# Kernel tuning notes

Measured on AMD Instinct MI355X. Metric: run time of the kernel, lower is better.

The kernel has to match this reference:

```python
import jax, jax.numpy as jnp
import numpy as np

NUM_NODES = 50000
NUM_EDGES = 800000
NUM_FEATS = 128
HIDDEN = 32
HEADS = 4
NUM_GRAPHS = 64
NEG_SLOPE = 0.2


def _glorot(key, shape):
    fan = shape[0] + shape[-1]
    return jax.random.normal(key, shape, jnp.float32) * np.float32(np.sqrt(2.0 / fan))


def setup_inputs() -> dict:
    key = jax.random.key(0)
    ks = jax.random.split(key, 16)
    x = jax.random.normal(ks[0], (NUM_NODES, NUM_FEATS), jnp.float32)
    edge_index = jax.random.randint(ks[1], (2, NUM_EDGES), 0, NUM_NODES, dtype=jnp.int64)
    batch = jnp.sort(jax.random.randint(ks[2], (NUM_NODES,), 0, NUM_GRAPHS, dtype=jnp.int64))
    d1 = HEADS * HIDDEN  # 128
    return {
        "x": x,
        "edge_index": edge_index,
        "batch": batch,
        # conv1: GATv2Conv(NUM_FEATS -> HIDDEN, heads=HEADS)
        "w1l": _glorot(ks[3], (d1, NUM_FEATS)),
        "b1l": jnp.zeros((d1,), jnp.float32),
        "w1r": _glorot(ks[4], (d1, NUM_FEATS)),
        "b1r": jnp.zeros((d1,), jnp.float32),
        "att1": _glorot(ks[5], (HEADS, HIDDEN)),
        "bias1": jnp.zeros((d1,), jnp.float32),
        # conv2: GATv2Conv(d1 -> HIDDEN, heads=1)
        "w2l": _glorot(ks[6], (HIDDEN, d1)),
        "b2l": jnp.zeros((HIDDEN,), jnp.float32),
        "w2r": _glorot(ks[7], (HIDDEN, d1)),
        "b2r": jnp.zeros((HIDDEN,), jnp.float32),
        "att2": _glorot(ks[8], (1, HIDDEN)),
        "bias2": jnp.zeros((HIDDEN,), jnp.float32),
        # output heads
        "wc": _glorot(ks[9], (1, HIDDEN)),
        "bc": jnp.zeros((1,), jnp.float32),
        "wp": _glorot(ks[10], (1, HIDDEN)),
        "bp": jnp.zeros((1,), jnp.float32),
    }


def gatv2_conv(x, wl, bl, wr, br, att, bias, src, dst, heads, ch):
    """PyG GATv2Conv (inference): gather, LeakyReLU score, scatter-softmax, scatter-add."""
    n = x.shape[0]
    xl = (x @ wl.T + bl).reshape(n, heads, ch)  # source-side transform
    xr = (x @ wr.T + br).reshape(n, heads, ch)  # target-side transform
    # per-edge pre-activation, [E, H, C]
    e = jax.nn.leaky_relu(xl[src] + xr[dst], NEG_SLOPE)
    score = jnp.einsum("ehc,hc->eh", e, att)  # [E, H]
    # scatter-softmax over incoming edges of each dst node (self-loops guarantee non-empty)
    smax = jax.ops.segment_max(score, dst, num_segments=n)
    ex = jnp.exp(score - smax[dst])
    denom = jax.ops.segment_sum(ex, dst, num_segments=n)
    alpha = ex / (denom[dst] + 1e-16)  # [E, H]
    out = jax.ops.segment_sum(xl[src] * alpha[:, :, None], dst, num_segments=n)  # [N, H, C]
    return out.reshape(n, heads * ch) + bias


def _forward(x, edge_index, batch,
             w1l, b1l, w1r, b1r, att1, bias1,
             w2l, b2l, w2r, b2r, att2, bias2,
             wc, bc, wp, bp):
    n = x.shape[0]
    # add self loops (PyG default add_self_loops=True)
    loop = jnp.arange(n, dtype=edge_index.dtype)
    src = jnp.concatenate([edge_index[0], loop])
    dst = jnp.concatenate([edge_index[1], loop])
    h = gatv2_conv(x, w1l, b1l, w1r, b1r, att1, bias1, src, dst, HEADS, HIDDEN)
    h = jax.nn.elu(h)
    # dropout is identity at inference
    h = gatv2_conv(h, w2l, b2l, w2r, b2r, att2, bias2, src, dst, 1, HIDDEN)
    h = jax.nn.elu(h)
    # global mean pool over graphs in the batch
    sums = jax.ops.segment_sum(h, batch, num_segments=NUM_GRAPHS)  # [G, HIDDEN]
    cnts = jax.ops.segment_sum(jnp.ones((n,), h.dtype), batch, num_segments=NUM_GRAPHS)
    pooled = sums / jnp.maximum(cnts, 1.0)[:, None]
    out_class = pooled @ wc.T + bc  # [G, 1]
    out_pseudo = pooled @ wp.T + bp  # [G, 1]
    return out_class, out_pseudo


def reference(x, edge_index, batch,
              w1l, b1l, w1r, b1r, att1, bias1,
              w2l, b2l, w2r, b2r, att2, bias2,
              wc, bc, wp, bp):
    return _forward(x, edge_index, batch,
                    w1l, b1l, w1r, b1r, att1, bias1,
                    w2l, b2l, w2r, b2r, att2, bias2,
                    wc, bc, wp, bp)
```

## Files before the change

kernel.cpp:

```cpp
#include <hip/hip_runtime.h>

#define N_NODES 50000
#define N_EDGES 800000
#define FEATS   128
#define HID     32
#define HEADS   4
#define D1      128
#define NGRAPH  64
#define SCAN_NB ((N_NODES + 1023) / 1024)

__device__ __forceinline__ float lrelu_(float v) { return fmaxf(v, 0.2f * v); }
__device__ __forceinline__ float elu_(float v)   { return v > 0.f ? v : __expf(v) - 1.f; }

typedef __attribute__((ext_vector_type(8))) short short8v;
typedef __attribute__((ext_vector_type(4))) float f32x4;
typedef _Float16 hv2 __attribute__((ext_vector_type(2)));

__device__ __forceinline__ unsigned short bf16hi_(float x) {
    unsigned u = __float_as_uint(x);
    unsigned r = u + 0x7FFFu + ((u >> 16) & 1);
    return (unsigned short)(r >> 16);
}
__device__ __forceinline__ float bf16f_(unsigned short h) {
    return __uint_as_float(((unsigned)h) << 16);
}

__device__ __forceinline__ hv2 h2mk_(float x, float y) {
    hv2 r; r.x = (_Float16)x; r.y = (_Float16)y; return r;
}
__device__ __forceinline__ float dot2acc_(hv2 a, hv2 b, float c) {
#if __has_builtin(__builtin_amdgcn_fdot2)
    return __builtin_amdgcn_fdot2(a, b, c, false);
#else
    return fmaf((float)a.x, (float)b.x, fmaf((float)a.y, (float)b.y, c));
#endif
}
__device__ __forceinline__ hv2 lrelu2_(hv2 t, hv2 c02) {
    return __builtin_elementwise_max(t, t * c02);
}
__device__ __forceinline__ unsigned short f2h_(float v) {
    return __builtin_bit_cast(unsigned short, (_Float16)v);
}

__global__ __launch_bounds__(256) void k_prep(
    const float* __restrict__ w1l, const float* __restrict__ w1r,
    unsigned short* __restrict__ bh, unsigned short* __restrict__ blo,
    const float* __restrict__ w2l, const float* __restrict__ w2r, float* __restrict__ wtg2,
    int* __restrict__ deg,
    const int* __restrict__ batch, int* __restrict__ gstart)
{
    int b = blockIdx.x;
    if (b < 128) {
        int idx = b * 256 + threadIdx.x;
        int j    = idx & 7;
        int lane = (idx >> 3) & 63;
        int ks   = (idx >> 9) & 3;
        int nfg  = idx >> 11;
        int col  = nfg * 16 + (lane & 15);
        int k    = ks * 32 + ((lane >> 4) & 3) * 8 + j;
        float wv = (col < 128) ? w1l[col * FEATS + k] : w1r[(col - 128) * FEATS + k];
        unsigned short h = bf16hi_(wv);
        float lo = wv - bf16f_(h);
        bh[idx]  = h;
        blo[idx] = bf16hi_(lo);
    } else if (b < 160) {
        int idx = (b - 128) * 256 + threadIdx.x;
        int kk = idx & 3, j = (idx >> 2) & 63, k4 = idx >> 8;
        int k = k4 * 4 + kk;
        wtg2[idx] = (j < 32) ? w2l[j * D1 + k] : w2r[(j - 32) * D1 + k];
    } else if (b < 356) {
        int i = (b - 160) * 256 + threadIdx.x;
        if (i < N_NODES) deg[i] = 0;
    } else {
        int i = (b - 356) * 256 + threadIdx.x;
        if (i > N_NODES) return;
        int bb   = (i < N_NODES) ? batch[i] : NGRAPH;
        int prev = (i == 0) ? -1 : batch[i - 1];
        for (int g = prev + 1; g <= bb; ++g) gstart[g] = i;
    }
}

__global__ __launch_bounds__(256) void k_hist(const int* __restrict__ ei,
                                              int* __restrict__ deg,
                                              int* __restrict__ rank)
{
    int e = blockIdx.x * 256 + threadIdx.x;
    if (e < N_EDGES) rank[e] = atomicAdd(&deg[ei[N_EDGES + e]], 1);
}

__global__ __launch_bounds__(1024) void k_scan_local(
    const int* __restrict__ deg, int* __restrict__ rs, int* __restrict__ btot)
{
    __shared__ int sm[1024];
    int idx = blockIdx.x * 1024 + threadIdx.x;
    int v = (idx < N_NODES) ? deg[idx] : 0;
    sm[threadIdx.x] = v;
    __syncthreads();
    for (int off = 1; off < 1024; off <<= 1) {
        int t = (threadIdx.x >= off) ? sm[threadIdx.x - off] : 0;
        __syncthreads();
        sm[threadIdx.x] += t;
        __syncthreads();
    }
    if (idx < N_NODES) rs[idx] = sm[threadIdx.x] - v;
    if (threadIdx.x == 1023) btot[blockIdx.x] = sm[1023];
}

__global__ __launch_bounds__(64) void k_scan_btot(
    const int* __restrict__ btot, int* __restrict__ boff)
{
    int t = threadIdx.x;
    int own = (t < SCAN_NB) ? btot[t] : 0;
    int v = own;
    for (int off = 1; off < 64; off <<= 1) {
        int u = __shfl_up(v, off);
        if (t >= off) v += u;
    }
    if (t < SCAN_NB) boff[t] = v - own;
}

__global__ __launch_bounds__(1024) void k_scan_add(
    int* __restrict__ rs, const int* __restrict__ boff)
{
    int idx = blockIdx.x * 1024 + threadIdx.x;
    if (idx < N_NODES) rs[idx] += boff[blockIdx.x];
    if (idx == N_NODES) rs[N_NODES] = N_EDGES;
}

__global__ __launch_bounds__(256) void k_scatter(const int* __restrict__ ei,
                                                const int* __restrict__ rs,
                                                const int* __restrict__ rank,
                                                int* __restrict__ csr_src)
{
    int e = blockIdx.x * 256 + threadIdx.x;
    if (e >= N_EDGES) return;
    int d = ei[N_EDGES + e];
    csr_src[rs[d] + rank[e]] = ei[e];
}

__global__ __launch_bounds__(256) void k_transform1(
    const float* __restrict__ x,
    const unsigned short* __restrict__ bh1, const unsigned short* __restrict__ bl1,
    const float* __restrict__ bl, const float* __restrict__ br,
    unsigned short* __restrict__ xlb, float* __restrict__ xr)
{
    __shared__ unsigned short XH[64 * 136];
    __shared__ unsigned short XL[64 * 136];
    int m0 = blockIdx.x * 64;
    for (int i = threadIdx.x; i < 2048; i += 256) {
        int r = i >> 5, c4 = i & 31;
        int n = m0 + r; if (n > N_NODES - 1) n = N_NODES - 1;
        float4 v = *(const float4*)&x[(size_t)n * FEATS + c4 * 4];
        ushort4 h, lo;
        h.x = bf16hi_(v.x); lo.x = bf16hi_(v.x - bf16f_(h.x));
        h.y = bf16hi_(v.y); lo.y = bf16hi_(v.y - bf16f_(h.y));
        h.z = bf16hi_(v.z); lo.z = bf16hi_(v.z - bf16f_(h.z));
        h.w = bf16hi_(v.w); lo.w = bf16hi_(v.w - bf16f_(h.w));
        *(ushort4*)&XH[r * 136 + c4 * 4] = h;
        *(ushort4*)&XL[r * 136 + c4 * 4] = lo;
    }
    __syncthreads();

    int l  = threadIdx.x & 63;
    int wq = threadIdx.x >> 6;
    int lr = l & 15;
    int lk = (l >> 4) & 3;

    f32x4 acc[4][4];
#pragma unroll
    for (int m = 0; m < 4; ++m)
#pragma unroll
        for (int n = 0; n < 4; ++n)
#pragma unroll
            for (int g = 0; g < 4; ++g) acc[m][n][g] = 0.f;

    const short8v* bhp = (const short8v*)bh1;
    const short8v* blp = (const short8v*)bl1;

#pragma unroll
    for (int ks = 0; ks < 4; ++ks) {
        short8v bh[4], bw[4], ah[4], al[4];
#pragma unroll
        for (int nf = 0; nf < 4; ++nf) {
            int fidx = (((wq * 4 + nf) * 4 + ks) * 64) + l;
            bh[nf] = bhp[fidx];
            bw[nf] = blp[fidx];
        }
#pragma unroll
        for (int mf = 0; mf < 4; ++mf) {
            int off = (mf * 16 + lr) * 136 + ks * 32 + lk * 8;
            ah[mf] = *(const short8v*)&XH[off];
            al[mf] = *(const short8v*)&XL[off];
        }
#pragma unroll
        for (int mf = 0; mf < 4; ++mf)
#pragma unroll
            for (int nf = 0; nf < 4; ++nf) {
                acc[mf][nf] = __builtin_amdgcn_mfma_f32_16x16x32_bf16(ah[mf], bh[nf], acc[mf][nf], 0, 0, 0);
                acc[mf][nf] = __builtin_amdgcn_mfma_f32_16x16x32_bf16(ah[mf], bw[nf], acc[mf][nf], 0, 0, 0);
                acc[mf][nf] = __builtin_amdgcn_mfma_f32_16x16x32_bf16(al[mf], bh[nf], acc[mf][nf], 0, 0, 0);
            }
    }

#pragma unroll
    for (int nf = 0; nf < 4; ++nf) {
        int col = wq * 64 + nf * 16 + lr;
        float bv = (col < 128) ? bl[col] : br[col - 128];
#pragma unroll
        for (int mf = 0; mf < 4; ++mf)
#pragma unroll
            for (int g = 0; g < 4; ++g) {
                int row = m0 + mf * 16 + lk * 4 + g;
                if (row > N_NODES - 1) row = N_NODES - 1;
                float v = acc[mf][nf][g] + bv;
                if (col < 128) xlb[(size_t)row * 128 + col] = f2h_(v);
                else           xr [(size_t)row * D1 + (col - 128)] = v;
            }
    }
}

__global__ __launch_bounds__(256, 2) void k_transform2(
    const float* __restrict__ hin, const float* __restrict__ wtg,
    const float* __restrict__ bl, const float* __restrict__ br,
    unsigned short* __restrict__ xlb2, float* __restrict__ xr2)
{
    __shared__ float4 xs[64][32];
    int node0 = blockIdx.x * 64;
    for (int i = threadIdx.x; i < 2048; i += 256) {
        int r = i >> 5, k4 = i & 31;
        int n = node0 + r; if (n > N_NODES - 1) n = N_NODES - 1;
        xs[r][k4] = *(const float4*)&hin[(size_t)n * D1 + k4 * 4];
    }
    __syncthreads();
    int j  = threadIdx.x & 31;
    int r0 = (threadIdx.x >> 5) * 8;
    const float4* __restrict__ wp = (const float4*)wtg;
    float accl[8], accr[8];
#pragma unroll
    for (int r = 0; r < 8; ++r) { accl[r] = 0.f; accr[r] = 0.f; }

    float4 wl_ = wp[j], wr_ = wp[j + 32];

#pragma unroll 2
    for (int k4 = 0; k4 < 32; ++k4) {
        int k4n = (k4 < 31) ? k4 + 1 : 31;
        float4 wln = wp[k4n * 64 + j];
        float4 wrn = wp[k4n * 64 + j + 32];
        float4 xv[8];
#pragma unroll
        for (int r = 0; r < 8; ++r) xv[r] = xs[r0 + r][k4];
#pragma unroll
        for (int r = 0; r < 8; ++r) {
            accl[r] = fmaf(wl_.x, xv[r].x, fmaf(wl_.y, xv[r].y,
                      fmaf(wl_.z, xv[r].z, fmaf(wl_.w, xv[r].w, accl[r]))));
            accr[r] = fmaf(wr_.x, xv[r].x, fmaf(wr_.y, xv[r].y,
                      fmaf(wr_.z, xv[r].z, fmaf(wr_.w, xv[r].w, accr[r]))));
        }
        wl_ = wln; wr_ = wrn;
    }
    float bls = bl[j], brs = br[j];
#pragma unroll
    for (int r = 0; r < 8; ++r) {
        int nn = node0 + r0 + r; if (nn > N_NODES - 1) nn = N_NODES - 1;
        size_t n = (size_t)nn;
        xlb2[n * HID + j] = f2h_(accl[r] + bls);
        xr2 [n * HID + j] = accr[r] + brs;
    }
}

__global__ __launch_bounds__(256) void k_gat1_fused(
    const int* __restrict__ rs, const int* __restrict__ csr_src,
    const unsigned short* __restrict__ xlb, const float* __restrict__ xr,
    const float* __restrict__ att, const float* __restrict__ bias,
    float* __restrict__ hout)
{
    int n = (blockIdx.x * 256 + threadIdx.x) >> 6;
    if (n >= N_NODES) return;
    int lane = threadIdx.x & 63;
    int d0   = lane & 31;
    int half = lane >> 5;
    const ushort4* xlp = (const ushort4*)xlb;
    float4 rf = ((const float4*)xr)[(size_t)n * 32 + d0];
    hv2 r01 = h2mk_(rf.x, rf.y), r23 = h2mk_(rf.z, rf.w);
    float4 af = ((const float4*)att)[d0];
    hv2 a01 = h2mk_(af.x, af.y), a23 = h2mk_(af.z, af.w);
    const hv2 c02 = h2mk_(0.2f, 0.2f);

    float den;
    float4 acc;
    {
        ushort4 lu = xlp[(size_t)n * 32 + d0];
        hv2 l01 = *(hv2*)&lu.x, l23 = *(hv2*)&lu.z;
        float sc = dot2acc_(lrelu2_(l01 + r01, c02), a01,
                   dot2acc_(lrelu2_(l23 + r23, c02), a23, 0.f));
        sc += __shfl_xor(sc, 1);
        sc += __shfl_xor(sc, 2);
        sc += __shfl_xor(sc, 4);
        float ex = (half == 0) ? __expf(sc) : 0.f;
        den = ex;
        acc.x = ex * (float)l01.x;  acc.y = ex * (float)l01.y;
        acc.z = ex * (float)l23.x;  acc.w = ex * (float)l23.y;
    }
    int e0 = rs[n], e1 = rs[n + 1];
    int p = e0;
    for (; p + 8 <= e1; p += 8) {
        int     sA[4];
        ushort4 lu[4];
        float   sb[4];
#pragma unroll
        for (int i = 0; i < 4; ++i) sA[i] = csr_src[p + 2 * i + half];
#pragma unroll
        for (int i = 0; i < 4; ++i) lu[i] = xlp[(size_t)sA[i] * 32 + d0];
        hv2 l01[4], l23[4];
#pragma unroll
        for (int i = 0; i < 4; ++i) { l01[i] = *(hv2*)&lu[i].x; l23[i] = *(hv2*)&lu[i].z; }
#pragma unroll
        for (int i = 0; i < 4; ++i)
            sb[i] = dot2acc_(lrelu2_(l01[i] + r01, c02), a01,
                    dot2acc_(lrelu2_(l23[i] + r23, c02), a23, 0.f));
#pragma unroll
        for (int i = 0; i < 4; ++i) sb[i] += __shfl_xor(sb[i], 1);
#pragma unroll
        for (int i = 0; i < 4; ++i) sb[i] += __shfl_xor(sb[i], 2);
#pragma unroll
        for (int i = 0; i < 4; ++i) sb[i] += __shfl_xor(sb[i], 4);
#pragma unroll
        for (int i = 0; i < 4; ++i) {
            float exx = __expf(sb[i]);
            den   += exx;
            acc.x += exx * (float)l01[i].x;
            acc.y += exx * (float)l01[i].y;
            acc.z += exx * (float)l23[i].x;
            acc.w += exx * (float)l23[i].y;
        }
    }
    for (; p < e1; p += 2) {
        int  idx = p + half;
        bool v   = idx < e1;
        int  s   = csr_src[v ? idx : e1 - 1];
        ushort4 lu = xlp[(size_t)s * 32 + d0];
        hv2 l01 = *(hv2*)&lu.x, l23 = *(hv2*)&lu.z;
        float s1 = dot2acc_(lrelu2_(l01 + r01, c02), a01,
                   dot2acc_(lrelu2_(l23 + r23, c02), a23, 0.f));
        s1 += __shfl_xor(s1, 1);
        s1 += __shfl_xor(s1, 2);
        s1 += __shfl_xor(s1, 4);
        float exx = v ? __expf(s1) : 0.f;
        den   += exx;
        acc.x += exx * (float)l01.x;
        acc.y += exx * (float)l01.y;
        acc.z += exx * (float)l23.x;
        acc.w += exx * (float)l23.y;
    }
    den   += __shfl_xor(den, 32);
    acc.x += __shfl_xor(acc.x, 32);
    acc.y += __shfl_xor(acc.y, 32);
    acc.z += __shfl_xor(acc.z, 32);
    acc.w += __shfl_xor(acc.w, 32);
    if (half == 0) {
        float inv = 1.f / (den + 1e-16f);
        float4 b = ((const float4*)bias)[d0];
        float4 o;
        o.x = elu_(acc.x * inv + b.x);
        o.y = elu_(acc.y * inv + b.y);
        o.z = elu_(acc.z * inv + b.z);
        o.w = elu_(acc.w * inv + b.w);
        ((float4*)hout)[(size_t)n * 32 + d0] = o;
    }
}

__global__ __launch_bounds__(256) void k_gat2_fused(
    const int* __restrict__ rs, const int* __restrict__ csr_src,
    const unsigned short* __restrict__ xlb2, const float* __restrict__ xr2,
    const float* __restrict__ att, const float* __restrict__ bias,
    float* __restrict__ h2)
{
    int n = (blockIdx.x * 256 + threadIdx.x) >> 5;
    if (n >= N_NODES) return;
    int lane = threadIdx.x & 31;
    int d0   = lane & 7;
    int sub  = lane >> 3;
    const ushort4* xlp = (const ushort4*)xlb2;
    float4 rf = ((const float4*)xr2)[(size_t)n * 8 + d0];
    hv2 r01 = h2mk_(rf.x, rf.y), r23 = h2mk_(rf.z, rf.w);
    float4 af = ((const float4*)att)[d0];
    hv2 a01 = h2mk_(af.x, af.y), a23 = h2mk_(af.z, af.w);
    const hv2 c02 = h2mk_(0.2f, 0.2f);

    float den;
    float4 acc;
    {
        ushort4 lu = xlp[(size_t)n * 8 + d0];
        hv2 l01 = *(hv2*)&lu.x, l23 = *(hv2*)&lu.z;
        float sc = dot2acc_(lrelu2_(l01 + r01, c02), a01,
                   dot2acc_(lrelu2_(l23 + r23, c02), a23, 0.f));
        sc += __shfl_xor(sc, 1);
        sc += __shfl_xor(sc, 2);
        sc += __shfl_xor(sc, 4);
        float ex = (sub == 0) ? __expf(sc) : 0.f;
        den = ex;
        acc.x = ex * (float)l01.x;  acc.y = ex * (float)l01.y;
        acc.z = ex * (float)l23.x;  acc.w = ex * (float)l23.y;
    }
    int e0 = rs[n], e1 = rs[n + 1];
    int p = e0;
    for (; p + 16 <= e1; p += 16) {
        int     sA[4];
        ushort4 lu[4];
        float   sb[4];
#pragma unroll
        for (int i = 0; i < 4; ++i) sA[i] = csr_src[p + 4 * i + sub];
#pragma unroll
        for (int i = 0; i < 4; ++i) lu[i] = xlp[(size_t)sA[i] * 8 + d0];
        hv2 l01[4], l23[4];
#pragma unroll
        for (int i = 0; i < 4; ++i) { l01[i] = *(hv2*)&lu[i].x; l23[i] = *(hv2*)&lu[i].z; }
#pragma unroll
        for (int i = 0; i < 4; ++i)
            sb[i] = dot2acc_(lrelu2_(l01[i] + r01, c02), a01,
                    dot2acc_(lrelu2_(l23[i] + r23, c02), a23, 0.f));
#pragma unroll
        for (int i = 0; i < 4; ++i) sb[i] += __shfl_xor(sb[i], 1);
#pragma unroll
        for (int i = 0; i < 4; ++i) sb[i] += __shfl_xor(sb[i], 2);
#pragma unroll
        for (int i = 0; i < 4; ++i) sb[i] += __shfl_xor(sb[i], 4);
#pragma unroll
        for (int i = 0; i < 4; ++i) {
            float exx = __expf(sb[i]);
            den   += exx;
            acc.x += exx * (float)l01[i].x;
            acc.y += exx * (float)l01[i].y;
            acc.z += exx * (float)l23[i].x;
            acc.w += exx * (float)l23[i].y;
        }
    }
    for (; p < e1; p += 4) {
        int  idx = p + sub;
        bool v   = idx < e1;
        int  s   = csr_src[v ? idx : e1 - 1];
        ushort4 lu = xlp[(size_t)s * 8 + d0];
        hv2 l01 = *(hv2*)&lu.x, l23 = *(hv2*)&lu.z;
        float s1 = dot2acc_(lrelu2_(l01 + r01, c02), a01,
                   dot2acc_(lrelu2_(l23 + r23, c02), a23, 0.f));
        s1 += __shfl_xor(s1, 1);
        s1 += __shfl_xor(s1, 2);
        s1 += __shfl_xor(s1, 4);
        float exx = v ? __expf(s1) : 0.f;
        den   += exx;
        acc.x += exx * (float)l01.x;
        acc.y += exx * (float)l01.y;
        acc.z += exx * (float)l23.x;
        acc.w += exx * (float)l23.y;
    }
    den   += __shfl_xor(den, 8);
    den   += __shfl_xor(den, 16);
    acc.x += __shfl_xor(acc.x, 8);  acc.x += __shfl_xor(acc.x, 16);
    acc.y += __shfl_xor(acc.y, 8);  acc.y += __shfl_xor(acc.y, 16);
    acc.z += __shfl_xor(acc.z, 8);  acc.z += __shfl_xor(acc.z, 16);
    acc.w += __shfl_xor(acc.w, 8);  acc.w += __shfl_xor(acc.w, 16);
    if (sub == 0) {
        float inv = 1.f / (den + 1e-16f);
        float4 b = ((const float4*)bias)[d0];
        float4 o;
        o.x = elu_(acc.x * inv + b.x);
        o.y = elu_(acc.y * inv + b.y);
        o.z = elu_(acc.z * inv + b.z);
        o.w = elu_(acc.w * inv + b.w);
        ((float4*)h2)[(size_t)n * 8 + d0] = o;
    }
}

__global__ __launch_bounds__(256) void k_pool_heads(
    const float* __restrict__ h2, const int* __restrict__ gstart,
    const float* __restrict__ wc, const float* __restrict__ bc,
    const float* __restrict__ wp, const float* __restrict__ bp,
    float* __restrict__ out)
{
    int g  = blockIdx.x;
    int n0 = gstart[g], n1 = gstart[g + 1];
    int c    = threadIdx.x & 31;
    int slot = threadIdx.x >> 5;
    float s = 0.f;
    for (int n = n0 + slot; n < n1; n += 8)
        s += h2[n * HID + c];
    __shared__ float red[8][HID];
    red[slot][c] = s;
    __syncthreads();
    if (slot == 0) {
        float tot = 0.f;
#pragma unroll
        for (int i = 0; i < 8; ++i) tot += red[i][c];
        float cntf = fmaxf((float)(n1 - n0), 1.f);
        float p = tot / cntf;
        float sc = p * wc[c];
        float sp = p * wp[c];
        sc += __shfl_xor(sc, 1);  sp += __shfl_xor(sp, 1);
        sc += __shfl_xor(sc, 2);  sp += __shfl_xor(sp, 2);
        sc += __shfl_xor(sc, 4);  sp += __shfl_xor(sp, 4);
        sc += __shfl_xor(sc, 8);  sp += __shfl_xor(sp, 8);
        sc += __shfl_xor(sc, 16); sp += __shfl_xor(sp, 16);
        if (c == 0) {
            out[g]          = sc + bc[0];
            out[NGRAPH + g] = sp + bp[0];
        }
    }
}

extern "C" void kernel_launch(void* const* d_in, const int* in_sizes, int n_in,
                              void* d_out, int out_size, void* d_ws, size_t ws_size,
                              hipStream_t stream)
{
    const float* x     = (const float*)d_in[0];
    const int*   ei    = (const int*)d_in[1];
    const int*   batch = (const int*)d_in[2];
    const float* w1l   = (const float*)d_in[3];
    const float* b1l   = (const float*)d_in[4];
    const float* w1r   = (const float*)d_in[5];
    const float* b1r   = (const float*)d_in[6];
    const float* att1  = (const float*)d_in[7];
    const float* bias1 = (const float*)d_in[8];
    const float* w2l   = (const float*)d_in[9];
    const float* b2l   = (const float*)d_in[10];
    const float* w2r   = (const float*)d_in[11];
    const float* b2r   = (const float*)d_in[12];
    const float* att2  = (const float*)d_in[13];
    const float* bias2 = (const float*)d_in[14];
    const float* wc    = (const float*)d_in[15];
    const float* bc    = (const float*)d_in[16];
    const float* wp    = (const float*)d_in[17];
    const float* bp    = (const float*)d_in[18];
    float* out = (float*)d_out;

    float* ws   = (float*)d_ws;
    unsigned short* xlb = (unsigned short*)ws;
    float* xr1  = ws + 6400000;
    float* hbuf = ws + 6400000;
    int* rank = (int*)(ws + 3200000);
    unsigned short* xlb2 = (unsigned short*)ws;
    float* xr2  = ws + 1600000;
    float* h2   = ws + 3200000;
    int* ibase   = (int*)(ws + 12800000);
    int* deg     = ibase;
    int* rs      = ibase + 50000;
    int* csr_src = ibase + 150001;
    int* gstart  = ibase + 950001;
    int* btot    = ibase + 950101;
    int* boff    = ibase + 950151;
    unsigned short* bh1 = (unsigned short*)(ws + 13800000);
    unsigned short* bl1_ = (unsigned short*)(ws + 13816384);
    float* wtg2 = ws + 13840000;

    k_prep<<<552, 256, 0, stream>>>(w1l, w1r, bh1, bl1_, w2l, w2r, wtg2, deg, batch, gstart);
    k_hist<<<(N_EDGES + 255) / 256, 256, 0, stream>>>(ei, deg, rank);
    k_scan_local<<<SCAN_NB, 1024, 0, stream>>>(deg, rs, btot);
    k_scan_btot<<<1, 64, 0, stream>>>(btot, boff);
    k_scan_add<<<SCAN_NB, 1024, 0, stream>>>(rs, boff);
    k_scatter<<<(N_EDGES + 255) / 256, 256, 0, stream>>>(ei, rs, rank, csr_src);

    k_transform1<<<(N_NODES + 63) / 64, 256, 0, stream>>>(x, bh1, bl1_, b1l, b1r, xlb, xr1);
    k_gat1_fused<<<(N_NODES * 64 + 255) / 256, 256, 0, stream>>>(rs, csr_src, xlb, xr1, att1, bias1, hbuf);

    k_transform2<<<(N_NODES + 63) / 64, 256, 0, stream>>>(hbuf, wtg2, b2l, b2r, xlb2, xr2);
    k_gat2_fused<<<(N_NODES * 32 + 255) / 256, 256, 0, stream>>>(rs, csr_src, xlb2, xr2, att2, bias2, h2);

    k_pool_heads<<<NGRAPH, 256, 0, stream>>>(h2, gstart, wc, bc, wp, bp, out);
}
```

Baseline: 202.5 us.

## Merge layer-1 transform with degree histogram and unroll GAT1 edge loop by 16

Fuses the layer-1 node transform and the edge-degree histogram into one launch, with extra blocks doing the atomic histogram. The two independent phases can then overlap on the GPU and one kernel launch is removed. It also adds a 16-edge unrolled gather loop ahead of the existing 8-edge loop in the layer-1 attention kernel, so more gathers are in flight per thread. The costs are more register pressure and a shared-memory allocation in the histogram blocks that they do not use, which may lower occupancy.

Measured after the change: 201.5 us. Within noise of the previous version (-0.5%).

```diff
diff --git a/kernel.cpp b/kernel.cpp
--- a/kernel.cpp
+++ b/kernel.cpp
@@ -8,6 +8,8 @@
 #define D1      128
 #define NGRAPH  64
 #define SCAN_NB ((N_NODES + 1023) / 1024)
+#define T1_NB   ((N_NODES + 63) / 64)
+#define HIST_NB ((N_EDGES + 255) / 256)
 
 __device__ __forceinline__ float lrelu_(float v) { return fmaxf(v, 0.2f * v); }
 __device__ __forceinline__ float elu_(float v)   { return v > 0.f ? v : __expf(v) - 1.f; }
@@ -80,72 +82,22 @@
     }
 }
 
-__global__ __launch_bounds__(256) void k_hist(const int* __restrict__ ei,
-                                              int* __restrict__ deg,
-                                              int* __restrict__ rank)
-{
-    int e = blockIdx.x * 256 + threadIdx.x;
-    if (e < N_EDGES) rank[e] = atomicAdd(&deg[ei[N_EDGES + e]], 1);
-}
-
-__global__ __launch_bounds__(1024) void k_scan_local(
-    const int* __restrict__ deg, int* __restrict__ rs, int* __restrict__ btot)
-{
-    __shared__ int sm[1024];
-    int idx = blockIdx.x * 1024 + threadIdx.x;
-    int v = (idx < N_NODES) ? deg[idx] : 0;
-    sm[threadIdx.x] = v;
-    __syncthreads();
-    for (int off = 1; off < 1024; off <<= 1) {
-        int t = (threadIdx.x >= off) ? sm[threadIdx.x - off] : 0;
-        __syncthreads();
-        sm[threadIdx.x] += t;
-        __syncthreads();
-    }
-    if (idx < N_NODES) rs[idx] = sm[threadIdx.x] - v;
-    if (threadIdx.x == 1023) btot[blockIdx.x] = sm[1023];
-}
-
-__global__ __launch_bounds__(64) void k_scan_btot(
-    const int* __restrict__ btot, int* __restrict__ boff)
-{
-    int t = threadIdx.x;
-    int own = (t < SCAN_NB) ? btot[t] : 0;
-    int v = own;
-    for (int off = 1; off < 64; off <<= 1) {
-        int u = __shfl_up(v, off);
-        if (t >= off) v += u;
-    }
-    if (t < SCAN_NB) boff[t] = v - own;
-}
-
-__global__ __launch_bounds__(1024) void k_scan_add(
-    int* __restrict__ rs, const int* __restrict__ boff)
-{
-    int idx = blockIdx.x * 1024 + threadIdx.x;
-    if (idx < N_NODES) rs[idx] += boff[blockIdx.x];
-    if (idx == N_NODES) rs[N_NODES] = N_EDGES;
-}
-
-__global__ __launch_bounds__(256) void k_scatter(const int* __restrict__ ei,
-                                                const int* __restrict__ rs,
-                                                const int* __restrict__ rank,
-                                                int* __restrict__ csr_src)
-{
-    int e = blockIdx.x * 256 + threadIdx.x;
-    if (e >= N_EDGES) return;
-    int d = ei[N_EDGES + e];
-    csr_src[rs[d] + rank[e]] = ei[e];
-}
-
-__global__ __launch_bounds__(256) void k_transform1(
+__global__ __launch_bounds__(256) void k_t1_hist(
     const float* __restrict__ x,
     const unsigned short* __restrict__ bh1, const unsigned short* __restrict__ bl1,
     const float* __restrict__ bl, const float* __restrict__ br,
-    unsigned short* __restrict__ xlb, float* __restrict__ xr)
+    unsigned short* __restrict__ xlb, float* __restrict__ xr,
+    const int* __restrict__ ei, int* __restrict__ deg, int* __restrict__ rank)
 {
     __shared__ unsigned short XH[64 * 136];
     __shared__ unsigned short XL[64 * 136];
+
+    if (blockIdx.x >= T1_NB) {
+        int e = (blockIdx.x - T1_NB) * 256 + threadIdx.x;
+        if (e < N_EDGES) rank[e] = atomicAdd(&deg[ei[N_EDGES + e]], 1);
+        return;
+    }
+
     int m0 = blockIdx.x * 64;
     for (int i = threadIdx.x; i < 2048; i += 256) {
         int r = i >> 5, c4 = i & 31;
@@ -217,6 +169,56 @@
                 else           xr [(size_t)row * D1 + (col - 128)] = v;
             }
     }
+}
+
+__global__ __launch_bounds__(1024) void k_scan_local(
+    const int* __restrict__ deg, int* __restrict__ rs, int* __restrict__ btot)
+{
+    __shared__ int sm[1024];
+    int idx = blockIdx.x * 1024 + threadIdx.x;
+    int v = (idx < N_NODES) ? deg[idx] : 0;
+    sm[threadIdx.x] = v;
+    __syncthreads();
+    for (int off = 1; off < 1024; off <<= 1) {
+        int t = (threadIdx.x >= off) ? sm[threadIdx.x - off] : 0;
+        __syncthreads();
+        sm[threadIdx.x] += t;
+        __syncthreads();
+    }
+    if (idx < N_NODES) rs[idx] = sm[threadIdx.x] - v;
+    if (threadIdx.x == 1023) btot[blockIdx.x] = sm[1023];
+}
+
+__global__ __launch_bounds__(64) void k_scan_btot(
+    const int* __restrict__ btot, int* __restrict__ boff)
+{
+    int t = threadIdx.x;
+    int own = (t < SCAN_NB) ? btot[t] : 0;
+    int v = own;
+    for (int off = 1; off < 64; off <<= 1) {
+        int u = __shfl_up(v, off);
+        if (t >= off) v += u;
+    }
+    if (t < SCAN_NB) boff[t] = v - own;
+}
+
+__global__ __launch_bounds__(1024) void k_scan_add(
+    int* __restrict__ rs, const int* __restrict__ boff)
+{
+    int idx = blockIdx.x * 1024 + threadIdx.x;
+    if (idx < N_NODES) rs[idx] += boff[blockIdx.x];
+    if (idx == N_NODES) rs[N_NODES] = N_EDGES;
+}
+
+__global__ __launch_bounds__(256) void k_scatter(const int* __restrict__ ei,
+                                                const int* __restrict__ rs,
+                                                const int* __restrict__ rank,
+                                                int* __restrict__ csr_src)
+{
+    int e = blockIdx.x * 256 + threadIdx.x;
+    if (e >= N_EDGES) return;
+    int d = ei[N_EDGES + e];
+    csr_src[rs[d] + rank[e]] = ei[e];
 }
 
 __global__ __launch_bounds__(256, 2) void k_transform2(
@@ -303,6 +305,37 @@
     }
     int e0 = rs[n], e1 = rs[n + 1];
     int p = e0;
+    for (; p + 16 <= e1; p += 16) {
+        int     sA[8];
+        ushort4 lu[8];
+        float   sb[8];
+#pragma unroll
+        for (int i = 0; i < 8; ++i) sA[i] = csr_src[p + 2 * i + half];
+#pragma unroll
+        for (int i = 0; i < 8; ++i) lu[i] = xlp[(size_t)sA[i] * 32 + d0];
+        hv2 l01[8], l23[8];
+#pragma unroll
+        for (int i = 0; i < 8; ++i) { l01[i] = *(hv2*)&lu[i].x; l23[i] = *(hv2*)&lu[i].z; }
+#pragma unroll
+        for (int i = 0; i < 8; ++i)
+            sb[i] = dot2acc_(lrelu2_(l01[i] + r01, c02), a01,
+                    dot2acc_(lrelu2_(l23[i] + r23, c02), a23, 0.f));
+#pragma unroll
+        for (int i = 0; i < 8; ++i) sb[i] += __shfl_xor(sb[i], 1);
+#pragma unroll
+        for (int i = 0; i < 8; ++i) sb[i] += __shfl_xor(sb[i], 2);
+#pragma unroll
+        for (int i = 0; i < 8; ++i) sb[i] += __shfl_xor(sb[i], 4);
+#pragma unroll
+        for (int i = 0; i < 8; ++i) {
+            float exx = __expf(sb[i]);
+            den   += exx;
+            acc.x += exx * (float)l01[i].x;
+            acc.y += exx * (float)l01[i].y;
+            acc.z += exx * (float)l23[i].x;
+            acc.w += exx * (float)l23[i].y;
+        }
+    }
     for (; p + 8 <= e1; p += 8) {
         int     sA[4];
         ushort4 lu[4];
@@ -552,13 +585,12 @@
     float* wtg2 = ws + 13840000;
 
     k_prep<<<552, 256, 0, stream>>>(w1l, w1r, bh1, bl1_, w2l, w2r, wtg2, deg, batch, gstart);
-    k_hist<<<(N_EDGES + 255) / 256, 256, 0, stream>>>(ei, deg, rank);
+    k_t1_hist<<<T1_NB + HIST_NB, 256, 0, stream>>>(x, bh1, bl1_, b1l, b1r, xlb, xr1, ei, deg, rank);
     k_scan_local<<<SCAN_NB, 1024, 0, stream>>>(deg, rs, btot);
     k_scan_btot<<<1, 64, 0, stream>>>(btot, boff);
     k_scan_add<<<SCAN_NB, 1024, 0, stream>>>(rs, boff);
     k_scatter<<<(N_EDGES + 255) / 256, 256, 0, stream>>>(ei, rs, rank, csr_src);
 
-    k_transform1<<<(N_NODES + 63) / 64, 256, 0, stream>>>(x, bh1, bl1_, b1l, b1r, xlb, xr1);
     k_gat1_fused<<<(N_NODES * 64 + 255) / 256, 256, 0, stream>>>(rs, csr_src, xlb, xr1, att1, bias1, hbuf);
 
     k_transform2<<<(N_NODES + 63) / 64, 256, 0, stream>>>(hbuf, wtg2, b2l, b2r, xlb2, xr2);
```
